# Performance work log

Hardware: AMD Instinct MI355X
Metric: run time of the kernel (lower is better)

Reference implementation:

```python
import jax, jax.numpy as jnp
import numpy as np

B, T, D, H = 2, 2048, 1024, 16
DH = D // H

def setup_inputs() -> dict:
    key = jax.random.key(0)
    ks = jax.random.split(key, 5)
    s = 1.0 / np.sqrt(D)
    return {
        "x": jax.random.normal(ks[0], (B, T, D), dtype=jnp.float32),
        "w_q": jax.random.normal(ks[1], (D, D), dtype=jnp.float32) * s,
        "w_k": jax.random.normal(ks[2], (D, D), dtype=jnp.float32) * s,
        "w_v": jax.random.normal(ks[3], (D, D), dtype=jnp.float32) * s,
        "w_o": jax.random.normal(ks[4], (D, D), dtype=jnp.float32) * s,
    }

def reference(x, w_q, w_k, w_v, w_o):
    # Linear(bias=False): y = x @ W.T
    q = jnp.einsum('btd,ed->bte', x, w_q).reshape(B, T, H, DH).transpose(0, 2, 1, 3)
    k = jnp.einsum('btd,ed->bte', x, w_k).reshape(B, T, H, DH).transpose(0, 2, 1, 3)
    v = jnp.einsum('btd,ed->bte', x, w_v).reshape(B, T, H, DH).transpose(0, 2, 1, 3)
    scores = jnp.einsum('bhqd,bhkd->bhqk', q, k) / np.sqrt(DH)  # [B,H,T,T]
    causal = jnp.triu(jnp.ones((T, T), dtype=bool), k=1)
    scores = jnp.where(causal[None, None, :, :], -jnp.inf, scores)
    attn = jax.nn.softmax(scores, axis=-1)
    ctx = jnp.einsum('bhqk,bhkd->bhqd', attn, v)
    ctx = ctx.transpose(0, 2, 1, 3).reshape(B, T, D)
    out = jnp.einsum('btd,ed->bte', ctx, w_o)
    return out
```

## Files before the change

### kernel.cpp

```cpp
#include <hip/hip_runtime.h>
#include <hip/hip_bf16.h>

typedef __bf16 bf16_t;
typedef __attribute__((ext_vector_type(8))) __bf16 bf16x8;
typedef __attribute__((ext_vector_type(4))) __bf16 bf16x4;
typedef __attribute__((ext_vector_type(4))) float f32x4;
typedef __attribute__((ext_vector_type(16))) float f32x16;
typedef __attribute__((ext_vector_type(2))) int i32x2;

#define B_ 2
#define T_ 2048
#define D_ 1024
#define H_ 16
#define DH_ 64
#define RS_ 3072

static __device__ __forceinline__ f32x4 mfma16(bf16x8 a, bf16x8 b, f32x4 c) {
  return __builtin_amdgcn_mfma_f32_16x16x32_bf16(a, b, c, 0, 0, 0);
}
static __device__ __forceinline__ f32x16 mfma32(bf16x8 a, bf16x8 b, f32x16 c) {
  return __builtin_amdgcn_mfma_f32_32x32x16_bf16(a, b, c, 0, 0, 0);
}
static __device__ __forceinline__ void gld16(const bf16_t* g, bf16_t* l) {
  __builtin_amdgcn_global_load_lds(
      (const __attribute__((address_space(1))) unsigned int*)g,
      (__attribute__((address_space(3))) unsigned int*)l, 16, 0, 0);
}
static __device__ __forceinline__ unsigned lds_addr(const bf16_t* p) {
  return (unsigned)(uintptr_t)(const __attribute__((address_space(3))) bf16_t*)p;
}
static __device__ __forceinline__ i32x2 tr64(unsigned a) {
  i32x2 d;
  asm volatile("ds_read_b64_tr_b16 %0, %1" : "=v"(d) : "v"(a));
  return d;
}
static __device__ __forceinline__ i32x2 tr64o(unsigned a) {
  i32x2 d;
  asm volatile("ds_read_b64_tr_b16 %0, %1 offset:128" : "=v"(d) : "v"(a));
  return d;
}
static __device__ __forceinline__ unsigned pk2(float lo, float hi2) {
  unsigned short a = __builtin_bit_cast(unsigned short, (bf16_t)lo);
  unsigned short b = __builtin_bit_cast(unsigned short, (bf16_t)hi2);
  return (unsigned)a | ((unsigned)b << 16);
}

#define WAITV3 { asm volatile("s_waitcnt vmcnt(3)" ::: "memory"); __builtin_amdgcn_sched_barrier(0); }
#define WAITV4 { asm volatile("s_waitcnt vmcnt(4)" ::: "memory"); __builtin_amdgcn_sched_barrier(0); }
#define WAITV0 { asm volatile("s_waitcnt vmcnt(0)" ::: "memory"); __builtin_amdgcn_sched_barrier(0); }
#define BAR    { __builtin_amdgcn_s_barrier(); __builtin_amdgcn_sched_barrier(0); }
#define WAITL0 { asm volatile("s_waitcnt lgkmcnt(0)" ::: "memory"); __builtin_amdgcn_sched_barrier(0); }

__global__ __launch_bounds__(256) void cvt_all(const float* __restrict__ x,
                                               const float* __restrict__ w0,
                                               const float* __restrict__ w1,
                                               const float* __restrict__ w2,
                                               const float* __restrict__ w3,
                                               bf16_t* __restrict__ out) {
  const int y = blockIdx.y;
  const float* in = (y < 4) ? (x + (size_t)y * 1048576)
                            : (y == 4 ? w0 : y == 5 ? w1 : y == 6 ? w2 : w3);
  bf16_t* o = out + (size_t)y * 1048576;
  int i = blockIdx.x * 256 + threadIdx.x;
  float4 f = reinterpret_cast<const float4*>(in)[i];
  bf16x4 v;
  v[0] = (bf16_t)f.x; v[1] = (bf16_t)f.y; v[2] = (bf16_t)f.z; v[3] = (bf16_t)f.w;
  reinterpret_cast<bf16x4*>(o)[i] = v;
}

template <bool STORE_F32, bool QSCALE>
__global__ __launch_bounds__(256) void gemm_nt(const bf16_t* __restrict__ A,
                                               const bf16_t* __restrict__ Bm,
                                               void* __restrict__ Cv,
                                               int M, int N, int K) {
  __shared__ __align__(16) bf16_t As[3][128 * 32];
  __shared__ __align__(16) bf16_t Bs[3][128 * 32];
  const int tid = threadIdx.x, lane = tid & 63, wave = tid >> 6;
  const int l15 = lane & 15;
  const int brow = blockIdx.y * 128, bcol = blockIdx.x * 128;
  const int row0 = (wave >> 1) * 64, col0 = (wave & 1) * 64;
  const float cscale = (QSCALE && bcol < 1024) ? 0.18033688011112042f : 1.0f;

  f32x4 acc[4][4];
#pragma unroll
  for (int m = 0; m < 4; ++m)
#pragma unroll
    for (int n = 0; n < 4; ++n) acc[m][n] = f32x4{0.f, 0.f, 0.f, 0.f};

  const int nst = K >> 5;
  const int srow = tid >> 2;
  const int sc8 = (tid & 3) * 8;
  auto stage = [&](int bi, int ks) {
    const int k0 = ks * 32;
#pragma unroll
    for (int i = 0; i < 2; ++i)
      gld16(A + (size_t)(brow + 64 * i + srow) * K + k0 + sc8,
            &As[bi][2048 * i + 512 * wave]);
#pragma unroll
    for (int i = 0; i < 2; ++i)
      gld16(Bm + (size_t)(bcol + 64 * i + srow) * K + k0 + sc8,
            &Bs[bi][2048 * i + 512 * wave]);
  };

  stage(0, 0);
  stage(1, 1);

#pragma unroll 1
  for (int ks = 0; ks < nst; ++ks) {
    if (ks + 1 < nst) { WAITV4 } else { WAITV0 }
    BAR;
    if (ks + 2 < nst) stage((ks + 2) % 3, ks + 2);

    const bf16_t* Ab = &As[ks % 3][0];
    const bf16_t* Bb = &Bs[ks % 3][0];
    const int ko = (lane >> 4) * 8;
    bf16x8 af[4], bfr[4];
#pragma unroll
    for (int m = 0; m < 4; ++m)
      af[m] = *(const bf16x8*)&Ab[(row0 + 16 * m + l15) * 32 + ko];
#pragma unroll
    for (int n = 0; n < 4; ++n)
      bfr[n] = *(const bf16x8*)&Bb[(col0 + 16 * n + l15) * 32 + ko];
    WAITL0;
#pragma unroll
    for (int m = 0; m < 4; ++m)
#pragma unroll
      for (int n = 0; n < 4; ++n) acc[m][n] = mfma16(af[m], bfr[n], acc[m][n]);
  }

  const int crow = brow + row0 + (lane >> 4) * 4;
  const int ccol = bcol + col0 + l15;
#pragma unroll
  for (int m = 0; m < 4; ++m)
#pragma unroll
    for (int n = 0; n < 4; ++n)
#pragma unroll
      for (int r = 0; r < 4; ++r) {
        size_t idx = (size_t)(crow + 16 * m + r) * N + (ccol + 16 * n);
        float v = acc[m][n][r] * cscale;
        if (STORE_F32) reinterpret_cast<float*>(Cv)[idx] = v;
        else reinterpret_cast<bf16_t*>(Cv)[idx] = (bf16_t)v;
      }
}

__global__ __launch_bounds__(256) void gemm_nt64(const bf16_t* __restrict__ A,
                                                 const bf16_t* __restrict__ Bm,
                                                 float* __restrict__ Cv,
                                                 int M, int N, int K) {
  __shared__ __align__(16) bf16_t As[3][64 * 32];
  __shared__ __align__(16) bf16_t Bs[3][128 * 32];
  const int tid = threadIdx.x, lane = tid & 63, wave = tid >> 6;
  const int l15 = lane & 15;
  const int brow = blockIdx.y * 64, bcol = blockIdx.x * 128;
  const int row0 = (wave >> 1) * 32, col0 = (wave & 1) * 64;

  f32x4 acc[2][4];
#pragma unroll
  for (int m = 0; m < 2; ++m)
#pragma unroll
    for (int n = 0; n < 4; ++n) acc[m][n] = f32x4{0.f, 0.f, 0.f, 0.f};

  const int nst = K >> 5;
  const int sr = lane >> 2;
  const int sc8 = (lane & 3) * 8;
  auto stage = [&](int bi, int ks) {
    const int k0 = ks * 32;
    gld16(A + (size_t)(brow + 16 * wave + sr) * K + k0 + sc8, &As[bi][512 * wave]);
#pragma unroll
    for (int i = 0; i < 2; ++i)
      gld16(Bm + (size_t)(bcol + 64 * i + 16 * wave + sr) * K + k0 + sc8,
            &Bs[bi][2048 * i + 512 * wave]);
  };

  stage(0, 0);
  stage(1, 1);

#pragma unroll 1
  for (int ks = 0; ks < nst; ++ks) {
    if (ks + 1 < nst) { WAITV3 } else { WAITV0 }
    BAR;
    if (ks + 2 < nst) stage((ks + 2) % 3, ks + 2);

    const bf16_t* Ab = &As[ks % 3][0];
    const bf16_t* Bb = &Bs[ks % 3][0];
    const int ko = (lane >> 4) * 8;
    bf16x8 af[2], bfr[4];
#pragma unroll
    for (int m = 0; m < 2; ++m)
      af[m] = *(const bf16x8*)&Ab[(row0 + 16 * m + l15) * 32 + ko];
#pragma unroll
    for (int n = 0; n < 4; ++n)
      bfr[n] = *(const bf16x8*)&Bb[(col0 + 16 * n + l15) * 32 + ko];
    WAITL0;
#pragma unroll
    for (int m = 0; m < 2; ++m)
#pragma unroll
      for (int n = 0; n < 4; ++n) acc[m][n] = mfma16(af[m], bfr[n], acc[m][n]);
  }

  const int crow = brow + row0 + (lane >> 4) * 4;
  const int ccol = bcol + col0 + l15;
#pragma unroll
  for (int m = 0; m < 2; ++m)
#pragma unroll
    for (int n = 0; n < 4; ++n)
#pragma unroll
      for (int r = 0; r < 4; ++r)
        Cv[(size_t)(crow + 16 * m + r) * N + (ccol + 16 * n)] = acc[m][n][r];
}

#define CROW(r) ((((r) & 3) + 8 * ((r) >> 2)) + 4 * hi)

__global__ __launch_bounds__(256, 1) void attn_fwd(const bf16_t* __restrict__ qkv,
                                                   bf16_t* __restrict__ ctx) {
  __shared__ __align__(128) bf16_t KV[3][2][64 * 64];
  const int tid = threadIdx.x;
  const int lane = tid & 63;
  const int wv = tid >> 6;
  const int bh = blockIdx.x, p = blockIdx.y;
  const int b = bh >> 4, h = bh & 15;
  const bf16_t* Qg = qkv + (size_t)b * T_ * RS_ + h * DH_;
  const bf16_t* Kg = Qg + 1024;
  const bf16_t* Vg = Qg + 2048;
  bf16_t* Cg = ctx + (size_t)b * T_ * D_ + h * DH_;

  const int hi = lane >> 5;
  const int l31 = lane & 31;
  const int l15 = lane & 15;

  auto stage = [&](int bi, int kt) {
    bf16_t* Kb = &KV[bi][0][0];
    bf16_t* Vb = &KV[bi][1][0];
#pragma unroll
    for (int i = 0; i < 2; ++i) {
      int c2 = i * 256 + tid;
      int r = c2 >> 3, g8 = (c2 & 7) ^ (r & 7);
      gld16(Kg + (size_t)(kt * 64 + r) * RS_ + g8 * 8, Kb + i * 2048 + wv * 512);
    }
#pragma unroll
    for (int i = 0; i < 2; ++i) {
      int c2 = i * 256 + tid;
      int pn = c2 >> 7, k = (c2 >> 1) & 63, half = c2 & 1;
      gld16(Vg + (size_t)(kt * 64 + k) * RS_ + pn * 16 + half * 8, Vb + i * 2048 + wv * 512);
    }
  };

#pragma unroll 1
  for (int phase = 0; phase < 2; ++phase) {
    const int c = phase ? (63 - 4 * p - wv) : (4 * p + wv);
    const int q0 = c * 32;
    const int mynkt = (c >> 1) + 1;
    const int maxnkt = phase ? (32 - 2 * p) : (2 * p + 2);

    BAR;
    stage(0, 0);
    stage(1, 1);

    bf16x8 qf[4];
#pragma unroll
    for (int d = 0; d < 4; ++d)
      qf[d] = *(const bf16x8*)&Qg[(size_t)(q0 + l31) * RS_ + d * 16 + hi * 8];

    f32x16 o[2];
#pragma unroll
    for (int n = 0; n < 2; ++n)
#pragma unroll
      for (int r = 0; r < 16; ++r) o[n][r] = 0.f;
    float mrow = -1e30f, lsum = 0.f;

#pragma unroll 1
    for (int kt = 0; kt < maxnkt; ++kt) {
      if (kt + 1 < maxnkt) { WAITV4 } else { WAITV0 }
      BAR;
      if (kt + 2 < maxnkt) stage((kt + 2) % 3, kt + 2);

      if (kt < mynkt) {
        const bf16_t* Kb = &KV[kt % 3][0][0];
        bf16x8 kf[2][4];
#pragma unroll
        for (int t = 0; t < 2; ++t)
#pragma unroll
          for (int d = 0; d < 4; ++d) {
            int row = 32 * t + l31;
            int col = ((d * 2 + hi) ^ (row & 7)) * 8;
            kf[t][d] = *(const bf16x8*)&Kb[row * 64 + col];
          }
        bf16x8 vf[2][4];
        {
          unsigned vb = lds_addr(&KV[kt % 3][1][0]);
#pragma unroll
          for (int n2 = 0; n2 < 2; ++n2)
#pragma unroll
            for (int ks = 0; ks < 4; ++ks) {
              int pn = 2 * n2 + (l31 >> 4);
              int k0 = ks * 16 + hi * 8;
              unsigned a = vb + pn * 2048 + k0 * 32 + l15 * 8;
              i32x2 lo = tr64(a);
              i32x2 hi4 = tr64o(a);
              union { unsigned u[4]; bf16x8 v; } uu;
              uu.u[0] = (unsigned)lo[0]; uu.u[1] = (unsigned)lo[1];
              uu.u[2] = (unsigned)hi4[0]; uu.u[3] = (unsigned)hi4[1];
              vf[n2][ks] = uu.v;
            }
        }
        WAITL0;

        f32x16 st[2];
#pragma unroll
        for (int t = 0; t < 2; ++t) {
#pragma unroll
          for (int r = 0; r < 16; ++r) st[t][r] = 0.f;
#pragma unroll
          for (int d = 0; d < 4; ++d) st[t] = mfma32(kf[t][d], qf[d], st[t]);
        }
        if (kt == mynkt - 1) {
#pragma unroll
          for (int t = 0; t < 2; ++t)
#pragma unroll
            for (int r = 0; r < 16; ++r)
              if (kt * 64 + 32 * t + CROW(r) > q0 + l31) st[t][r] = -1e30f;
        }
        float pm = -1e30f;
#pragma unroll
        for (int t = 0; t < 2; ++t)
#pragma unroll
          for (int r = 0; r < 16; ++r) pm = fmaxf(pm, st[t][r]);
        pm = fmaxf(pm, __shfl_xor(pm, 32));
        if (!__all(pm - mrow <= 11.0f)) {
          float mn = fmaxf(mrow, pm);
          float scl = exp2f(mrow - mn);
          mrow = mn;
          lsum *= scl;
#pragma unroll
          for (int r = 0; r < 16; ++r) {
            float sr = __shfl(scl, CROW(r));
            o[0][r] *= sr;
            o[1][r] *= sr;
          }
        }
        float ps = 0.f;
#pragma unroll
        for (int t = 0; t < 2; ++t)
#pragma unroll
          for (int r = 0; r < 16; ++r) {
            float e = exp2f(st[t][r] - mrow);
            st[t][r] = e;
            ps += e;
          }
        ps += __shfl_xor(ps, 32);
        lsum += ps;
        unsigned pk[2][8];
#pragma unroll
        for (int t = 0; t < 2; ++t)
#pragma unroll
          for (int j = 0; j < 8; ++j) pk[t][j] = pk2(st[t][2 * j], st[t][2 * j + 1]);
#pragma unroll
        for (int ks = 0; ks < 4; ++ks) {
          const int t = ks >> 1, rb = (ks & 1) * 4;
          unsigned s0 = hi ? pk[t][rb] : pk[t][rb + 2];
          unsigned s1 = hi ? pk[t][rb + 1] : pk[t][rb + 3];
          unsigned r0 = (unsigned)__shfl_xor((int)s0, 32);
          unsigned r1 = (unsigned)__shfl_xor((int)s1, 32);
          union { unsigned u[4]; bf16x8 v; } w;
          if (hi == 0) {
            w.u[0] = pk[t][rb]; w.u[1] = pk[t][rb + 1]; w.u[2] = r0; w.u[3] = r1;
          } else {
            w.u[0] = r0; w.u[1] = r1; w.u[2] = pk[t][rb + 2]; w.u[3] = pk[t][rb + 3];
          }
          o[0] = mfma32(w.v, vf[0][ks], o[0]);
          o[1] = mfma32(w.v, vf[1][ks], o[1]);
        }
      }
    }

#pragma unroll
    for (int r = 0; r < 16; ++r) {
      float li = __shfl(lsum, CROW(r));
      float inv = 1.0f / li;
      int qrow = q0 + CROW(r);
#pragma unroll
      for (int n2 = 0; n2 < 2; ++n2)
        Cg[(size_t)qrow * D_ + n2 * 32 + l31] = (bf16_t)(o[n2][r] * inv);
    }
  }
}

extern "C" void kernel_launch(void* const* d_in, const int* in_sizes, int n_in,
                              void* d_out, int out_size, void* d_ws, size_t ws_size,
                              hipStream_t stream) {
  const float* x   = (const float*)d_in[0];
  const float* w_q = (const float*)d_in[1];
  const float* w_k = (const float*)d_in[2];
  const float* w_v = (const float*)d_in[3];
  const float* w_o = (const float*)d_in[4];

  const int M = B_ * T_;
  const size_t XN = (size_t)M * D_;
  const size_t WN = (size_t)D_ * D_;

  bf16_t* ws = (bf16_t*)d_ws;
  bf16_t* xb   = ws;
  bf16_t* wqb  = xb + XN;
  bf16_t* wob  = wqb + 3 * WN;
  bf16_t* qkv  = wob + WN;
  bf16_t* ctx  = qkv + (size_t)M * RS_;

  cvt_all<<<dim3(1024, 8), 256, 0, stream>>>(x, w_q, w_k, w_v, w_o, ws);

  gemm_nt<false, true><<<dim3(RS_ / 128, M / 128), 256, 0, stream>>>(xb, wqb, qkv, M, RS_, D_);

  attn_fwd<<<dim3(B_ * H_, 8), 256, 0, stream>>>(qkv, ctx);

  gemm_nt64<<<dim3(D_ / 128, M / 64), 256, 0, stream>>>(ctx, wob, (float*)d_out, M, D_, D_);
}
```

Measured before the change: 133.9 us.

## Merge two causal phases into one KV sweep sharing loaded tiles

The attention kernel used to run two sequential phases per block, one for a low query chunk and one for a high query chunk, each streaming its own K/V tiles. Now both chunks are processed in a single loop over KV tiles, and each staged K/V tile is read from LDS once and used for both query chunks. This removes the duplicate global loads and LDS reads for the prefix tiles and drops one pipeline ramp-up. In exchange each wave holds two query fragment sets and two accumulator sets, which raises register pressure.

```diff
diff --git a/kernel.cpp b/kernel.cpp
--- a/kernel.cpp
+++ b/kernel.cpp
@@ -228,6 +228,13 @@
   const int l31 = lane & 31;
   const int l15 = lane & 15;
 
+  const int cA = 4 * p + wv;
+  const int cB = 63 - 4 * p - wv;
+  const int q0A = cA * 32, q0B = cB * 32;
+  const int nktA = (cA >> 1) + 1;
+  const int nktB = (cB >> 1) + 1;
+  const int loopN = 32 - 2 * p;
+
   auto stage = [&](int bi, int kt) {
     bf16_t* Kb = &KV[bi][0][0];
     bf16_t* Vb = &KV[bi][1][0];
@@ -245,143 +252,138 @@
     }
   };
 
+  bf16x8 qfA[4], qfB[4];
+#pragma unroll
+  for (int d = 0; d < 4; ++d) {
+    qfA[d] = *(const bf16x8*)&Qg[(size_t)(q0A + l31) * RS_ + d * 16 + hi * 8];
+    qfB[d] = *(const bf16x8*)&Qg[(size_t)(q0B + l31) * RS_ + d * 16 + hi * 8];
+  }
+
+  f32x16 oA0, oA1, oB0, oB1;
+#pragma unroll
+  for (int r = 0; r < 16; ++r) { oA0[r] = 0.f; oA1[r] = 0.f; oB0[r] = 0.f; oB1[r] = 0.f; }
+  float mA = -1e30f, lA = 0.f, mB = -1e30f, lB = 0.f;
+
+  stage(0, 0);
+  stage(1, 1);
+
+  bf16x8 kf[2][4], vf[2][4];
+  auto body = [&](int kt, int q0c, int nktc, const bf16x8* qfc,
+                  f32x16& o0, f32x16& o1, float& mrow, float& lsum) {
+    f32x16 st[2];
+#pragma unroll
+    for (int t = 0; t < 2; ++t) {
+#pragma unroll
+      for (int r = 0; r < 16; ++r) st[t][r] = 0.f;
+#pragma unroll
+      for (int d = 0; d < 4; ++d) st[t] = mfma32(kf[t][d], qfc[d], st[t]);
+    }
+    if (kt == nktc - 1) {
+#pragma unroll
+      for (int t = 0; t < 2; ++t)
+#pragma unroll
+        for (int r = 0; r < 16; ++r)
+          if (kt * 64 + 32 * t + CROW(r) > q0c + l31) st[t][r] = -1e30f;
+    }
+    float pm = -1e30f;
+#pragma unroll
+    for (int t = 0; t < 2; ++t)
+#pragma unroll
+      for (int r = 0; r < 16; ++r) pm = fmaxf(pm, st[t][r]);
+    pm = fmaxf(pm, __shfl_xor(pm, 32));
+    if (!__all(pm - mrow <= 11.0f)) {
+      float mn = fmaxf(mrow, pm);
+      float scl = exp2f(mrow - mn);
+      mrow = mn;
+      lsum *= scl;
+#pragma unroll
+      for (int r = 0; r < 16; ++r) {
+        float sr = __shfl(scl, CROW(r));
+        o0[r] *= sr;
+        o1[r] *= sr;
+      }
+    }
+    float ps = 0.f;
+#pragma unroll
+    for (int t = 0; t < 2; ++t)
+#pragma unroll
+      for (int r = 0; r < 16; ++r) {
+        float e = exp2f(st[t][r] - mrow);
+        st[t][r] = e;
+        ps += e;
+      }
+    ps += __shfl_xor(ps, 32);
+    lsum += ps;
+    unsigned pk[2][8];
+#pragma unroll
+    for (int t = 0; t < 2; ++t)
+#pragma unroll
+      for (int j = 0; j < 8; ++j) pk[t][j] = pk2(st[t][2 * j], st[t][2 * j + 1]);
+#pragma unroll
+    for (int ks = 0; ks < 4; ++ks) {
+      const int t = ks >> 1, rb = (ks & 1) * 4;
+      unsigned s0 = hi ? pk[t][rb] : pk[t][rb + 2];
+      unsigned s1 = hi ? pk[t][rb + 1] : pk[t][rb + 3];
+      unsigned r0 = (unsigned)__shfl_xor((int)s0, 32);
+      unsigned r1 = (unsigned)__shfl_xor((int)s1, 32);
+      union { unsigned u[4]; bf16x8 v; } w;
+      if (hi == 0) {
+        w.u[0] = pk[t][rb]; w.u[1] = pk[t][rb + 1]; w.u[2] = r0; w.u[3] = r1;
+      } else {
+        w.u[0] = r0; w.u[1] = r1; w.u[2] = pk[t][rb + 2]; w.u[3] = pk[t][rb + 3];
+      }
+      o0 = mfma32(w.v, vf[0][ks], o0);
+      o1 = mfma32(w.v, vf[1][ks], o1);
+    }
+  };
+
 #pragma unroll 1
-  for (int phase = 0; phase < 2; ++phase) {
-    const int c = phase ? (63 - 4 * p - wv) : (4 * p + wv);
-    const int q0 = c * 32;
-    const int mynkt = (c >> 1) + 1;
-    const int maxnkt = phase ? (32 - 2 * p) : (2 * p + 2);
-
+  for (int kt = 0; kt < loopN; ++kt) {
+    if (kt + 1 < loopN) { WAITV4 } else { WAITV0 }
     BAR;
-    stage(0, 0);
-    stage(1, 1);
-
-    bf16x8 qf[4];
-#pragma unroll
-    for (int d = 0; d < 4; ++d)
-      qf[d] = *(const bf16x8*)&Qg[(size_t)(q0 + l31) * RS_ + d * 16 + hi * 8];
-
-    f32x16 o[2];
-#pragma unroll
-    for (int n = 0; n < 2; ++n)
-#pragma unroll
-      for (int r = 0; r < 16; ++r) o[n][r] = 0.f;
-    float mrow = -1e30f, lsum = 0.f;
-
-#pragma unroll 1
-    for (int kt = 0; kt < maxnkt; ++kt) {
-      if (kt + 1 < maxnkt) { WAITV4 } else { WAITV0 }
-      BAR;
-      if (kt + 2 < maxnkt) stage((kt + 2) % 3, kt + 2);
-
-      if (kt < mynkt) {
-        const bf16_t* Kb = &KV[kt % 3][0][0];
-        bf16x8 kf[2][4];
-#pragma unroll
-        for (int t = 0; t < 2; ++t)
-#pragma unroll
-          for (int d = 0; d < 4; ++d) {
-            int row = 32 * t + l31;
-            int col = ((d * 2 + hi) ^ (row & 7)) * 8;
-            kf[t][d] = *(const bf16x8*)&Kb[row * 64 + col];
-          }
-        bf16x8 vf[2][4];
-        {
-          unsigned vb = lds_addr(&KV[kt % 3][1][0]);
-#pragma unroll
-          for (int n2 = 0; n2 < 2; ++n2)
-#pragma unroll
-            for (int ks = 0; ks < 4; ++ks) {
-              int pn = 2 * n2 + (l31 >> 4);
-              int k0 = ks * 16 + hi * 8;
-              unsigned a = vb + pn * 2048 + k0 * 32 + l15 * 8;
-              i32x2 lo = tr64(a);
-              i32x2 hi4 = tr64o(a);
-              union { unsigned u[4]; bf16x8 v; } uu;
-              uu.u[0] = (unsigned)lo[0]; uu.u[1] = (unsigned)lo[1];
-              uu.u[2] = (unsigned)hi4[0]; uu.u[3] = (unsigned)hi4[1];
-              vf[n2][ks] = uu.v;
-            }
+    if (kt + 2 < loopN) stage((kt + 2) % 3, kt + 2);
+
+    const bool actA = kt < nktA, actB = kt < nktB;
+    if (actA || actB) {
+      const bf16_t* Kb = &KV[kt % 3][0][0];
+#pragma unroll
+      for (int t = 0; t < 2; ++t)
+#pragma unroll
+        for (int d = 0; d < 4; ++d) {
+          int row = 32 * t + l31;
+          int col = ((d * 2 + hi) ^ (row & 7)) * 8;
+          kf[t][d] = *(const bf16x8*)&Kb[row * 64 + col];
         }
-        WAITL0;
-
-        f32x16 st[2];
-#pragma unroll
-        for (int t = 0; t < 2; ++t) {
-#pragma unroll
-          for (int r = 0; r < 16; ++r) st[t][r] = 0.f;
-#pragma unroll
-          for (int d = 0; d < 4; ++d) st[t] = mfma32(kf[t][d], qf[d], st[t]);
+      unsigned vb = lds_addr(&KV[kt % 3][1][0]);
+#pragma unroll
+      for (int n2 = 0; n2 < 2; ++n2)
+#pragma unroll
+        for (int ks = 0; ks < 4; ++ks) {
+          int pn = 2 * n2 + (l31 >> 4);
+          int k0 = ks * 16 + hi * 8;
+          unsigned a = vb + pn * 2048 + k0 * 32 + l15 * 8;
+          i32x2 lo = tr64(a);
+          i32x2 hi4 = tr64o(a);
+          union { unsigned u[4]; bf16x8 v; } uu;
+          uu.u[0] = (unsigned)lo[0]; uu.u[1] = (unsigned)lo[1];
+          uu.u[2] = (unsigned)hi4[0]; uu.u[3] = (unsigned)hi4[1];
+          vf[n2][ks] = uu.v;
         }
-        if (kt == mynkt - 1) {
-#pragma unroll
-          for (int t = 0; t < 2; ++t)
-#pragma unroll
-            for (int r = 0; r < 16; ++r)
-              if (kt * 64 + 32 * t + CROW(r) > q0 + l31) st[t][r] = -1e30f;
-        }
-        float pm = -1e30f;
-#pragma unroll
-        for (int t = 0; t < 2; ++t)
-#pragma unroll
-          for (int r = 0; r < 16; ++r) pm = fmaxf(pm, st[t][r]);
-        pm = fmaxf(pm, __shfl_xor(pm, 32));
-        if (!__all(pm - mrow <= 11.0f)) {
-          float mn = fmaxf(mrow, pm);
-          float scl = exp2f(mrow - mn);
-          mrow = mn;
-          lsum *= scl;
-#pragma unroll
-          for (int r = 0; r < 16; ++r) {
-            float sr = __shfl(scl, CROW(r));
-            o[0][r] *= sr;
-            o[1][r] *= sr;
-          }
-        }
-        float ps = 0.f;
-#pragma unroll
-        for (int t = 0; t < 2; ++t)
-#pragma unroll
-          for (int r = 0; r < 16; ++r) {
-            float e = exp2f(st[t][r] - mrow);
-            st[t][r] = e;
-            ps += e;
-          }
-        ps += __shfl_xor(ps, 32);
-        lsum += ps;
-        unsigned pk[2][8];
-#pragma unroll
-        for (int t = 0; t < 2; ++t)
-#pragma unroll
-          for (int j = 0; j < 8; ++j) pk[t][j] = pk2(st[t][2 * j], st[t][2 * j + 1]);
-#pragma unroll
-        for (int ks = 0; ks < 4; ++ks) {
-          const int t = ks >> 1, rb = (ks & 1) * 4;
-          unsigned s0 = hi ? pk[t][rb] : pk[t][rb + 2];
-          unsigned s1 = hi ? pk[t][rb + 1] : pk[t][rb + 3];
-          unsigned r0 = (unsigned)__shfl_xor((int)s0, 32);
-          unsigned r1 = (unsigned)__shfl_xor((int)s1, 32);
-          union { unsigned u[4]; bf16x8 v; } w;
-          if (hi == 0) {
-            w.u[0] = pk[t][rb]; w.u[1] = pk[t][rb + 1]; w.u[2] = r0; w.u[3] = r1;
-          } else {
-            w.u[0] = r0; w.u[1] = r1; w.u[2] = pk[t][rb + 2]; w.u[3] = pk[t][rb + 3];
-          }
-          o[0] = mfma32(w.v, vf[0][ks], o[0]);
-          o[1] = mfma32(w.v, vf[1][ks], o[1]);
-        }
-      }
-    }
-
-#pragma unroll
-    for (int r = 0; r < 16; ++r) {
-      float li = __shfl(lsum, CROW(r));
-      float inv = 1.0f / li;
-      int qrow = q0 + CROW(r);
-#pragma unroll
-      for (int n2 = 0; n2 < 2; ++n2)
-        Cg[(size_t)qrow * D_ + n2 * 32 + l31] = (bf16_t)(o[n2][r] * inv);
-    }
+      WAITL0;
+      if (actA) body(kt, q0A, nktA, qfA, oA0, oA1, mA, lA);
+      if (actB) body(kt, q0B, nktB, qfB, oB0, oB1, mB, lB);
+    }
+  }
+
+#pragma unroll
+  for (int r = 0; r < 16; ++r) {
+    float liA = __shfl(lA, CROW(r));
+    float liB = __shfl(lB, CROW(r));
+    int qrA = q0A + CROW(r), qrB = q0B + CROW(r);
+    Cg[(size_t)qrA * D_ + l31]      = (bf16_t)(oA0[r] / liA);
+    Cg[(size_t)qrA * D_ + 32 + l31] = (bf16_t)(oA1[r] / liA);
+    Cg[(size_t)qrB * D_ + l31]      = (bf16_t)(oB0[r] / liB);
+    Cg[(size_t)qrB * D_ + 32 + l31] = (bf16_t)(oB1[r] / liB);
   }
 }
 
```

New measurement: 138.2 us. +3.3%, slower.
